# Optimization experiments

Hardware: AMD Instinct MI355X
Metric: run time of the kernel (lower is better)

## Reference

```python
import jax, jax.numpy as jnp
import numpy as np

A, B, OBS, ACT, E, H = 8, 32768, 128, 32, 128, 4
D = E // H  # attend_dim = 32
EPS = 1e-5


def setup_inputs() -> dict:
    key = jax.random.key(0)
    ks = jax.random.split(key, 20)
    std = 0.02
    inp = {
        "observation_vector": jax.random.normal(ks[0], (A, B, OBS), jnp.float32),
        "action_vector": jax.random.uniform(ks[1], (A, B, ACT), jnp.float32),
        # per-agent BatchNorm affine params (torch default init would be 1/0; the
        # module re-inits everything N(0, 0.02), we just use standard BN init)
        "g_gamma": jnp.ones((A, OBS + ACT), jnp.float32),
        "g_beta": jnp.zeros((A, OBS + ACT), jnp.float32),
        "Wg": jax.random.normal(ks[2], (A, OBS + ACT, E), jnp.float32) * std,
        "bg": jnp.zeros((A, E), jnp.float32),
        "s_gamma": jnp.ones((A, OBS), jnp.float32),
        "s_beta": jnp.zeros((A, OBS), jnp.float32),
        "Ws": jax.random.normal(ks[3], (A, OBS, E), jnp.float32) * std,
        "bs": jnp.zeros((A, E), jnp.float32),
        # per-head attention projections (no bias)
        "Wq": jax.random.normal(ks[4], (H, E, D), jnp.float32) * std,
        "Wk": jax.random.normal(ks[5], (H, E, D), jnp.float32) * std,
        "Wv": jax.random.normal(ks[6], (H, E, D), jnp.float32) * std,
        # per-agent f-functions: Linear(2E -> E), LeakyReLU, Linear(E -> ACT)
        "Wf1": jax.random.normal(ks[7], (A, 2 * E, E), jnp.float32) * std,
        "bf1": jnp.zeros((A, E), jnp.float32),
        "Wf2": jax.random.normal(ks[8], (A, E, ACT), jnp.float32) * std,
        "bf2": jnp.zeros((A, ACT), jnp.float32),
    }
    return inp


def _bn(x, gamma, beta):
    # training-mode BatchNorm1d per agent: normalize over batch axis (axis=1)
    mean = x.mean(axis=1, keepdims=True)
    var = x.var(axis=1, keepdims=True)  # biased variance, as torch BN forward
    return (x - mean) * jax.lax.rsqrt(var + EPS) * gamma[:, None, :] + beta[:, None, :]


def reference(observation_vector, action_vector, g_gamma, g_beta, Wg, bg,
              s_gamma, s_beta, Ws, bs, Wq, Wk, Wv, Wf1, bf1, Wf2, bf2):
    lrelu = jax.nn.leaky_relu  # slope 0.01, matches torch default

    combined = jnp.concatenate([observation_vector, action_vector], axis=2)  # [A,B,OBS+ACT]
    e = lrelu(jnp.einsum('abf,afe->abe', _bn(combined, g_gamma, g_beta), Wg) + bg[:, None, :])  # [A,B,E]
    s = lrelu(jnp.einsum('abf,afe->abe', _bn(observation_vector, s_gamma, s_beta), Ws) + bs[:, None, :])  # [A,B,E]

    # per-head projections for all agents at once
    q = jnp.einsum('abe,hed->ahbd', e, Wq)          # [A,H,B,D]
    k = jnp.einsum('abe,hed->ahbd', e, Wk)          # [A,H,B,D]
    v = lrelu(jnp.einsum('abe,hed->ahbd', e, Wv))   # [A,H,B,D]

    # unnormalized scores alpha[i,j] = <k_j, q_i>/sqrt(D) (NO softmax in original)
    alpha = jnp.einsum('ihbd,jhbd->ijhb', q, k) / np.sqrt(D)  # [A,A,H,B]
    mask = 1.0 - jnp.eye(A, dtype=alpha.dtype)                 # exclude j == i
    total = jnp.einsum('ijhb,jhbd->ihbd', alpha * mask[:, :, None, None], v)  # [A,H,B,D]
    xi = jnp.transpose(total, (0, 2, 1, 3)).reshape(A, B, H * D)  # heads concatenated -> [A,B,E]

    fin = jnp.concatenate([xi, s], axis=2)  # [A,B,2E]
    h1 = lrelu(jnp.einsum('abf,afe->abe', fin, Wf1) + bf1[:, None, :])
    all_action_q = jnp.einsum('abe,aec->abc', h1, Wf2) + bf2[:, None, :]  # [A,B,ACT]

    action_ids = jnp.argmax(action_vector, axis=2)  # [A,B]
    curr_action_q = jnp.take_along_axis(all_action_q, action_ids[:, :, None], axis=2)  # [A,B,1]
    return curr_action_q
```

## Files before the change

### kernel.cpp

```cpp
#include <hip/hip_runtime.h>

#define A_ 8
#define B_ 32768
#define OBS_ 128
#define ACT_ 32
#define F_ 160
#define E_ 128
#define H_ 4
#define D_ 32
#define NB_ 16

typedef __attribute__((ext_vector_type(8))) short s16x8;
typedef __attribute__((ext_vector_type(4))) float f32x4;

__device__ __forceinline__ float bf2f(ushort u) {
    union { uint i; float f; } v; v.i = ((uint)u) << 16; return v.f;
}
__device__ __forceinline__ ushort f2bf(float x) {
    union { float f; uint i; } v; v.f = x;
    return (ushort)((v.i + 0x7FFF + ((v.i >> 16) & 1)) >> 16);
}
__device__ __forceinline__ float lrelu(float x) { return x > 0.f ? x : 0.01f * x; }

#define MFMA16(a, b, c) __builtin_amdgcn_mfma_f32_16x16x32_bf16((a), (b), (c), 0, 0, 0)

#define WSB_GSUM   0
#define WSB_GSQ    5120
#define WSB_MEAN   10240
#define WSB_RSTD   15360
#define WSB_BG2    20480
#define WSB_BS2    24576
#define WSB_WGT    28672
#define WSB_WSTH   356352
#define WSB_WSTL   618496
#define WSB_WQT    880640
#define WSB_WKT    913408
#define WSB_WVT    946176
#define WSB_WF1T   978944
#define WSB_WF1TL  1503232
#define WSB_WF2T   1765376
#define WSB_TOTAL  1896448

#define SLOT(m)     ((m) * 9728)
#define XHI(m,r,c)  (SLOT(m) + (r) * 336 + (c) * 2)
#define XLO(m,r,c)  (SLOT(m) + 5376 + (r) * 272 + (c) * 2)
#define SHI(m,r,c)  (SLOT(m) + (r) * 272 + (c) * 2)
#define SLO(m,r,c)  (SLOT(m) + 4352 + (r) * 272 + (c) * 2)
#define OFF_E   77824
#define EA(R,c) (OFF_E + (R) * 272 + (c) * 2)
#define OFF_V   112640
#define VA(R,c) (OFF_V + (R) * 256 + (c) * 2)
#define OFF_QH  145920
#define OFF_KH  150272
#define OFF_AL  154624
#define OFF_BI  162816
#define OFF_PART 163328
#define SMEM_BYTES 163840
__device__ __forceinline__ int qswz(int R, int cb) {
    int a = R * 32 + cb; return a ^ (((R >> 4) & 7) << 4);
}

__global__ void k_zero(float* __restrict__ p) {
    const int i = blockIdx.x * 256 + threadIdx.x;
    if (i < 2560) p[i] = 0.f;
}

__global__ __launch_bounds__(256) void k_stats(const float* __restrict__ obs,
                                               const float* __restrict__ act,
                                               float* __restrict__ gsum,
                                               float* __restrict__ gsq) {
    const int a = blockIdx.y;
    const int b0 = blockIdx.x * (B_ / 64);
    const int tid = threadIdx.x;
    __shared__ float red[256][8];

    {
        const int c = tid & 31, rg = tid >> 5;
        const float4* src = (const float4*)(obs + (size_t)a * B_ * OBS_);
        float4 s = make_float4(0.f,0.f,0.f,0.f), q = make_float4(0.f,0.f,0.f,0.f);
        for (int b = b0 + rg; b < b0 + 512; b += 8) {
            float4 v = src[(size_t)b * 32 + c];
            s.x += v.x; s.y += v.y; s.z += v.z; s.w += v.w;
            q.x += v.x*v.x; q.y += v.y*v.y; q.z += v.z*v.z; q.w += v.w*v.w;
        }
        red[tid][0]=s.x; red[tid][1]=s.y; red[tid][2]=s.z; red[tid][3]=s.w;
        red[tid][4]=q.x; red[tid][5]=q.y; red[tid][6]=q.z; red[tid][7]=q.w;
    }
    __syncthreads();
    if (tid < 128) {
        const int c4 = tid >> 2, j = tid & 3;
        float s = 0.f, q = 0.f;
        #pragma unroll
        for (int rg = 0; rg < 8; rg++) { s += red[rg*32 + c4][j]; q += red[rg*32 + c4][4 + j]; }
        atomicAdd(&gsum[a * F_ + tid], s);
        atomicAdd(&gsq [a * F_ + tid], q);
    }
    __syncthreads();
    {
        const int c = tid & 7, rg = tid >> 3;
        const float4* src = (const float4*)(act + (size_t)a * B_ * ACT_);
        float4 s = make_float4(0.f,0.f,0.f,0.f), q = make_float4(0.f,0.f,0.f,0.f);
        for (int b = b0 + rg; b < b0 + 512; b += 32) {
            float4 v = src[(size_t)b * 8 + c];
            s.x += v.x; s.y += v.y; s.z += v.z; s.w += v.w;
            q.x += v.x*v.x; q.y += v.y*v.y; q.z += v.z*v.z; q.w += v.w*v.w;
        }
        red[tid][0]=s.x; red[tid][1]=s.y; red[tid][2]=s.z; red[tid][3]=s.w;
        red[tid][4]=q.x; red[tid][5]=q.y; red[tid][6]=q.z; red[tid][7]=q.w;
    }
    __syncthreads();
    if (tid < 32) {
        const int c4 = tid >> 2, j = tid & 3;
        float s = 0.f, q = 0.f;
        #pragma unroll
        for (int rg = 0; rg < 32; rg++) { s += red[rg*8 + c4][j]; q += red[rg*8 + c4][4 + j]; }
        atomicAdd(&gsum[a * F_ + 128 + tid], s);
        atomicAdd(&gsq [a * F_ + 128 + tid], q);
    }
}

__global__ void k_finalize(const float* __restrict__ gsum, const float* __restrict__ gsq,
                           float* __restrict__ mean, float* __restrict__ rstd) {
    const int i = blockIdx.x * 256 + threadIdx.x;
    if (i < A_ * F_) {
        const float m = gsum[i] * (1.0f / B_);
        const float v = gsq[i] * (1.0f / B_) - m * m;
        mean[i] = m;
        rstd[i] = rsqrtf(v + 1e-5f);
    }
}

__global__ void k_fold_bias(const float* __restrict__ W, const float* __restrict__ gamma,
                            const float* __restrict__ beta, const float* __restrict__ bias,
                            const float* __restrict__ mean, const float* __restrict__ rstd,
                            float* __restrict__ b2, int F) {
    const int a = blockIdx.x;
    const int c = threadIdx.x;
    float acc = bias[a * E_ + c];
    for (int f = 0; f < F; f++) {
        const float coef = beta[a * F + f] - mean[a * F_ + f] * rstd[a * F_ + f] * gamma[a * F + f];
        acc += coef * W[((size_t)a * F + f) * E_ + c];
    }
    b2[a * E_ + c] = acc;
}

__global__ void k_prep_wgT(const float* __restrict__ Wg, const float* __restrict__ gg,
                           const float* __restrict__ rstd, ushort* __restrict__ WgT) {
    int i = blockIdx.x * 256 + threadIdx.x;
    if (i >= 8 * 128 * 160) return;
    int a = i / (128 * 160), rest = i % (128 * 160);
    int n = rest / 160, k = rest % 160;
    float w = Wg[((size_t)a * 160 + k) * 128 + n] * gg[a * 160 + k] * rstd[a * 160 + k];
    WgT[i] = f2bf(w);
}
__global__ void k_prep_wsT(const float* __restrict__ Ws, const float* __restrict__ sg,
                           const float* __restrict__ rstd,
                           ushort* __restrict__ Th, ushort* __restrict__ Tl) {
    int i = blockIdx.x * 256 + threadIdx.x;
    if (i >= 8 * 128 * 128) return;
    int a = i / (128 * 128), rest = i % (128 * 128);
    int n = rest / 128, k = rest % 128;
    float w = Ws[((size_t)a * 128 + k) * 128 + n] * sg[a * 128 + k] * rstd[a * 160 + k];
    ushort h = f2bf(w);
    Th[i] = h;
    Tl[i] = f2bf(w - bf2f(h));
}
__global__ void k_prep_qkvT(const float* __restrict__ Wq, const float* __restrict__ Wk,
                            const float* __restrict__ Wv, ushort* __restrict__ Tq,
                            ushort* __restrict__ Tk, ushort* __restrict__ Tv) {
    int i = blockIdx.x * 256 + threadIdx.x;
    if (i >= 4 * 32 * 128) return;
    int h = i / (32 * 128), rest = i % (32 * 128);
    int d = rest / 128, e = rest % 128;
    size_t src = ((size_t)h * 128 + e) * 32 + d;
    Tq[i] = f2bf(Wq[src]); Tk[i] = f2bf(Wk[src]); Tv[i] = f2bf(Wv[src]);
}
__global__ void k_prep_f1T(const float* __restrict__ Wf1, ushort* __restrict__ Th,
                           ushort* __restrict__ Tl) {
    int i = blockIdx.x * 256 + threadIdx.x;
    if (i >= 8 * 128 * 256) return;
    int a = i / (128 * 256), rest = i % (128 * 256);
    int n = rest / 256, k = rest % 256;
    float w = Wf1[((size_t)a * 256 + k) * 128 + n];
    ushort h = f2bf(w);
    Th[i] = h;
    if (k >= 128) Tl[((size_t)(a * 128 + n)) * 128 + (k - 128)] = f2bf(w - bf2f(h));
}
__global__ void k_prep_f2T(const float* __restrict__ Wf2, float* __restrict__ T) {
    int i = blockIdx.x * 256 + threadIdx.x;
    if (i >= 8 * 32 * 128) return;
    int a = i / (32 * 128), rest = i % (32 * 128);
    int c = rest / 128, k = rest % 128;
    T[i] = Wf2[((size_t)a * 128 + k) * 32 + c];
}

__global__ __launch_bounds__(512, 1) void k_fused(
    const float* __restrict__ obs, const float* __restrict__ act,
    const ushort* __restrict__ WgT, const float* __restrict__ bg2,
    const ushort* __restrict__ WsTh, const ushort* __restrict__ WsTl,
    const float* __restrict__ bs2,
    const ushort* __restrict__ WqT, const ushort* __restrict__ WkT,
    const ushort* __restrict__ WvT,
    const ushort* __restrict__ Wf1T, const ushort* __restrict__ Wf1Tl,
    const float* __restrict__ bf1,
    const float* __restrict__ Wf2T, const float* __restrict__ bfc2,
    float* __restrict__ out) {
    extern __shared__ char smc[];
    const int tid = threadIdx.x;
    const int b0 = blockIdx.x * NB_;
    const int lane = tid & 63, wv = tid >> 6;
    const int l16 = lane & 15, l4 = lane >> 4;

    {
        const int R = tid >> 2, q = tid & 3;
        const int a = R >> 4, r = R & 15;
        const float* ap = act + ((size_t)a * B_ + b0 + r) * 32 + q * 8;
        float bv = -1e30f; int bi = 0;
        #pragma unroll
        for (int u = 0; u < 8; u++) { float x = ap[u]; if (x > bv) { bv = x; bi = q * 8 + u; } }
        #pragma unroll
        for (int off = 1; off < 4; off <<= 1) {
            float ov = __shfl_xor(bv, off, 4);
            int   oi = __shfl_xor(bi, off, 4);
            if (ov > bv || (ov == bv && oi < bi)) { bv = ov; bi = oi; }
        }
        if (q == 0) *(int*)(smc + OFF_BI + R * 4) = bi;
    }

    for (int i = tid; i < 4096; i += 512) {
        const int R = i >> 5, c4 = i & 31;
        const int a = R >> 4, r = R & 15;
        float4 v = *(const float4*)(obs + ((size_t)a * B_ + b0 + r) * 128 + c4 * 4);
        float vv[4] = {v.x, v.y, v.z, v.w};
        #pragma unroll
        for (int j = 0; j < 4; j++) {
            ushort h = f2bf(vv[j]);
            *(ushort*)(smc + XHI(a, r, c4 * 4 + j)) = h;
            *(ushort*)(smc + XLO(a, r, c4 * 4 + j)) = f2bf(vv[j] - bf2f(h));
        }
    }
    for (int i = tid; i < 1024; i += 512) {
        const int R = i >> 3, c4 = i & 7;
        const int a = R >> 4, r = R & 15;
        float4 v = *(const float4*)(act + ((size_t)a * B_ + b0 + r) * 32 + c4 * 4);
        float vv[4] = {v.x, v.y, v.z, v.w};
        #pragma unroll
        for (int j = 0; j < 4; j++)
            *(ushort*)(smc + XHI(a, r, 128 + c4 * 4 + j)) = f2bf(vv[j]);
    }
    __syncthreads();

    const int n = wv * 16 + l16;

    {
        f32x4 acc[8];
        #pragma unroll
        for (int m = 0; m < 8; m++) acc[m] = (f32x4){0.f, 0.f, 0.f, 0.f};
        #pragma unroll
        for (int kc = 0; kc < 5; kc++) {
            const int kof = kc * 32 + l4 * 8;
            #pragma unroll
            for (int m = 0; m < 8; m++) {
                s16x8 a = *(const s16x8*)(smc + XHI(m, l16, kof));
                s16x8 b = *(const s16x8*)(WgT + ((size_t)m * 128 + n) * 160 + kof);
                acc[m] = MFMA16(a, b, acc[m]);
            }
        }
        #pragma unroll
        for (int m = 0; m < 8; m++) {
            const float bb = bg2[m * 128 + n];
            #pragma unroll
            for (int j = 0; j < 4; j++)
                *(ushort*)(smc + EA(m * 16 + l4 * 4 + j, n)) = f2bf(lrelu(acc[m][j] + bb));
        }
    }
    __syncthreads();

    for (int m = 0; m < 8; m++) {
        f32x4 acc = (f32x4){0.f, 0.f, 0.f, 0.f};
        #pragma unroll
        for (int kc = 0; kc < 4; kc++) {
            const int kof = kc * 32 + l4 * 8;
            s16x8 ah = *(const s16x8*)(smc + XHI(m, l16, kof));
            s16x8 al = *(const s16x8*)(smc + XLO(m, l16, kof));
            s16x8 bh = *(const s16x8*)(WsTh + ((size_t)m * 128 + n) * 128 + kof);
            s16x8 bl = *(const s16x8*)(WsTl + ((size_t)m * 128 + n) * 128 + kof);
            acc = MFMA16(ah, bh, acc);
            acc = MFMA16(al, bh, acc);
            acc = MFMA16(ah, bl, acc);
        }
        __syncthreads();
        const float bb = bs2[m * 128 + n];
        #pragma unroll
        for (int j = 0; j < 4; j++) {
            float s = lrelu(acc[j] + bb);
            ushort h = f2bf(s);
            *(ushort*)(smc + SHI(m, l4 * 4 + j, n)) = h;
            *(ushort*)(smc + SLO(m, l4 * 4 + j, n)) = f2bf(s - bf2f(h));
        }
    }

    {
        f32x4 acc[8];
        #pragma unroll
        for (int m = 0; m < 8; m++) acc[m] = (f32x4){0.f, 0.f, 0.f, 0.f};
        const int h = n >> 5, dl = n & 31;
        const ushort* wp = WvT + ((size_t)(h * 32 + dl)) * 128;
        #pragma unroll
        for (int kc = 0; kc < 4; kc++) {
            const int kof = kc * 32 + l4 * 8;
            s16x8 b = *(const s16x8*)(wp + kof);
            #pragma unroll
            for (int m = 0; m < 8; m++) {
                s16x8 a = *(const s16x8*)(smc + EA(m * 16 + l16, kof));
                acc[m] = MFMA16(a, b, acc[m]);
            }
        }
        #pragma unroll
        for (int m = 0; m < 8; m++)
            #pragma unroll
            for (int j = 0; j < 4; j++)
                *(ushort*)(smc + VA(m * 16 + l4 * 4 + j, n)) = f2bf(lrelu(acc[m][j]));
    }

    float da0 = 0.f, da1 = 0.f;
    for (int hh = 0; hh < 8; hh++) {
        const int h = hh >> 1, dh = hh & 1;
        {
            f32x4 aq = (f32x4){0.f, 0.f, 0.f, 0.f}, ak = (f32x4){0.f, 0.f, 0.f, 0.f};
            const int dl = dh * 16 + l16;
            const ushort* wq = WqT + ((size_t)(h * 32 + dl)) * 128;
            const ushort* wk = WkT + ((size_t)(h * 32 + dl)) * 128;
            #pragma unroll
            for (int kc = 0; kc < 4; kc++) {
                const int kof = kc * 32 + l4 * 8;
                s16x8 a  = *(const s16x8*)(smc + EA(wv * 16 + l16, kof));
                s16x8 bq = *(const s16x8*)(wq + kof);
                s16x8 bk = *(const s16x8*)(wk + kof);
                aq = MFMA16(a, bq, aq);
                ak = MFMA16(a, bk, ak);
            }
            __syncthreads();
            #pragma unroll
            for (int j = 0; j < 4; j++) {
                const int R = wv * 16 + l4 * 4 + j;
                *(ushort*)(smc + OFF_QH + qswz(R, l16 * 2)) = f2bf(aq[j]);
                *(ushort*)(smc + OFF_KH + qswz(R, l16 * 2)) = f2bf(ak[j]);
            }
        }
        __syncthreads();
        #pragma unroll
        for (int p = 0; p < 2; p++) {
            const int e = p * 512 + tid;
            const int j = e & 7, i = (e >> 3) & 7, r = e >> 6;
            const int Rq = i * 16 + r, Rk = j * 16 + r;
            s16x8 q0 = *(const s16x8*)(smc + OFF_QH + qswz(Rq, 0));
            s16x8 q1 = *(const s16x8*)(smc + OFF_QH + qswz(Rq, 16));
            s16x8 k0 = *(const s16x8*)(smc + OFF_KH + qswz(Rk, 0));
            s16x8 k1 = *(const s16x8*)(smc + OFF_KH + qswz(Rk, 16));
            float d = 0.f;
            #pragma unroll
            for (int u = 0; u < 8; u++) d += bf2f((ushort)q0[u]) * bf2f((ushort)k0[u]);
            #pragma unroll
            for (int u = 0; u < 8; u++) d += bf2f((ushort)q1[u]) * bf2f((ushort)k1[u]);
            float& da = p ? da1 : da0;
            if (dh == 0) da = d;
            else {
                const float tot = da + d;
                *(ushort*)(smc + OFF_AL + ((h * 16 + r) * 64 + i * 8 + j) * 2) =
                    (i == j) ? (ushort)0 : f2bf(tot * 0.17677669529663687f);
            }
        }
    }
    __syncthreads();

    for (int m = 0; m < 8; m++) {
        {
            const int c = tid & 127, rg = tid >> 7;
            const int h = c >> 5;
            #pragma unroll
            for (int rr = 0; rr < 4; rr++) {
                const int r = rg * 4 + rr;
                float acc = 0.f;
                #pragma unroll
                for (int j = 0; j < 8; j++) {
                    const float al = bf2f(*(const ushort*)(smc + OFF_AL + ((h * 16 + r) * 64 + m * 8 + j) * 2));
                    const float vv = bf2f(*(const ushort*)(smc + VA(j * 16 + r, c)));
                    acc += al * vv;
                }
                *(ushort*)(smc + EA(r, c)) = f2bf(acc);
            }
        }
        __syncthreads();
        {
            f32x4 acc = (f32x4){0.f, 0.f, 0.f, 0.f};
            const ushort* w1  = Wf1T  + ((size_t)m * 128 + n) * 256;
            const ushort* w1l = Wf1Tl + ((size_t)m * 128 + n) * 128;
            #pragma unroll
            for (int kc = 0; kc < 4; kc++) {
                const int kof = kc * 32 + l4 * 8;
                s16x8 a = *(const s16x8*)(smc + EA(l16, kof));
                s16x8 b = *(const s16x8*)(w1 + kof);
                acc = MFMA16(a, b, acc);
            }
            #pragma unroll
            for (int kc = 0; kc < 4; kc++) {
                const int kof = kc * 32 + l4 * 8;
                s16x8 ah = *(const s16x8*)(smc + SHI(m, l16, kof));
                s16x8 al = *(const s16x8*)(smc + SLO(m, l16, kof));
                s16x8 bh = *(const s16x8*)(w1 + 128 + kof);
                s16x8 bl = *(const s16x8*)(w1l + kof);
                acc = MFMA16(ah, bh, acc);
                acc = MFMA16(al, bh, acc);
                acc = MFMA16(ah, bl, acc);
            }
            const float bb = bf1[m * 128 + n];
            float ps[4];
            #pragma unroll
            for (int j = 0; j < 4; j++) {
                const int r = l4 * 4 + j;
                const int bi = *(const int*)(smc + OFF_BI + (m * 16 + r) * 4);
                const float w2 = Wf2T[((size_t)m * 32 + bi) * 128 + n];
                ps[j] = lrelu(acc[j] + bb) * w2;
            }
            #pragma unroll
            for (int off = 1; off < 16; off <<= 1)
                #pragma unroll
                for (int j = 0; j < 4; j++) ps[j] += __shfl_xor(ps[j], off, 16);
            if (l16 == 0)
                #pragma unroll
                for (int j = 0; j < 4; j++)
                    *(float*)(smc + OFF_PART + ((l4 * 4 + j) * 8 + wv) * 4) = ps[j];
        }
        __syncthreads();
        if (tid < 16) {
            float o = 0.f;
            #pragma unroll
            for (int w = 0; w < 8; w++) o += *(const float*)(smc + OFF_PART + (tid * 8 + w) * 4);
            const int bi = *(const int*)(smc + OFF_BI + (m * 16 + tid) * 4);
            out[(size_t)m * B_ + b0 + tid] = o + bfc2[m * 32 + bi];
        }
        __syncthreads();
    }
}

extern "C" void kernel_launch(void* const* d_in, const int* in_sizes, int n_in,
                              void* d_out, int out_size, void* d_ws, size_t ws_size,
                              hipStream_t stream) {
    const float* obs     = (const float*)d_in[0];
    const float* act     = (const float*)d_in[1];
    const float* g_gamma = (const float*)d_in[2];
    const float* g_beta  = (const float*)d_in[3];
    const float* Wg      = (const float*)d_in[4];
    const float* bg      = (const float*)d_in[5];
    const float* s_gamma = (const float*)d_in[6];
    const float* s_beta  = (const float*)d_in[7];
    const float* Ws      = (const float*)d_in[8];
    const float* bs      = (const float*)d_in[9];
    const float* Wq      = (const float*)d_in[10];
    const float* Wk      = (const float*)d_in[11];
    const float* Wv      = (const float*)d_in[12];
    const float* Wf1     = (const float*)d_in[13];
    const float* bf1     = (const float*)d_in[14];
    const float* Wf2     = (const float*)d_in[15];
    const float* bf2     = (const float*)d_in[16];

    if (ws_size < (size_t)WSB_TOTAL) return;

    (void)hipFuncSetAttribute((const void*)k_fused,
                              hipFuncAttributeMaxDynamicSharedMemorySize, SMEM_BYTES);

    char* ws = (char*)d_ws;
    float*  gsum  = (float*)(ws + WSB_GSUM);
    float*  gsq   = (float*)(ws + WSB_GSQ);
    float*  mean  = (float*)(ws + WSB_MEAN);
    float*  rstd  = (float*)(ws + WSB_RSTD);
    float*  bg2   = (float*)(ws + WSB_BG2);
    float*  bs2   = (float*)(ws + WSB_BS2);
    ushort* WgT   = (ushort*)(ws + WSB_WGT);
    ushort* WsTh  = (ushort*)(ws + WSB_WSTH);
    ushort* WsTl  = (ushort*)(ws + WSB_WSTL);
    ushort* WqT   = (ushort*)(ws + WSB_WQT);
    ushort* WkT   = (ushort*)(ws + WSB_WKT);
    ushort* WvT   = (ushort*)(ws + WSB_WVT);
    ushort* Wf1T  = (ushort*)(ws + WSB_WF1T);
    ushort* Wf1Tl = (ushort*)(ws + WSB_WF1TL);
    float*  Wf2T  = (float*)(ws + WSB_WF2T);

    k_zero<<<10, 256, 0, stream>>>(gsum);
    k_stats<<<dim3(64, A_), 256, 0, stream>>>(obs, act, gsum, gsq);
    k_finalize<<<5, 256, 0, stream>>>(gsum, gsq, mean, rstd);
    k_fold_bias<<<A_, 128, 0, stream>>>(Wg, g_gamma, g_beta, bg, mean, rstd, bg2, F_);
    k_fold_bias<<<A_, 128, 0, stream>>>(Ws, s_gamma, s_beta, bs, mean, rstd, bs2, OBS_);
    k_prep_wgT<<<640, 256, 0, stream>>>(Wg, g_gamma, rstd, WgT);
    k_prep_wsT<<<512, 256, 0, stream>>>(Ws, s_gamma, rstd, WsTh, WsTl);
    k_prep_qkvT<<<64, 256, 0, stream>>>(Wq, Wk, Wv, WqT, WkT, WvT);
    k_prep_f1T<<<1024, 256, 0, stream>>>(Wf1, Wf1T, Wf1Tl);
    k_prep_f2T<<<128, 256, 0, stream>>>(Wf2, Wf2T);
    k_fused<<<B_ / NB_, 512, SMEM_BYTES, stream>>>(
        obs, act, WgT, bg2, WsTh, WsTl, bs2, WqT, WkT, WvT,
        Wf1T, Wf1Tl, bf1, Wf2T, bf2, (float*)d_out);
}
```

Measured before the change: 1.048 ms.

## Restructure fused kernel: merge embedding GEMMs, per-head QK, per-agent f-layer ownership

Merges the Wg and Ws embedding GEMMs into a single pass over the shared input tiles, and computes Q/K one head at a time into swizzled shared buffers so all attention scores are built before aggregation. The value aggregation then runs in one pass, and each wave owns one agent for the f1/f2 layers, so output reductions stay within the wave and per-agent block barriers go away. It also spreads the batch-stats kernel over four times as many blocks. The restructuring trades extra registers (eight held accumulators) and new swizzle layouts for fewer __syncthreads and less redundant shared-memory traffic.

```diff
diff --git a/kernel.cpp b/kernel.cpp
--- a/kernel.cpp
+++ b/kernel.cpp
@@ -44,20 +44,23 @@
 #define SLOT(m)     ((m) * 9728)
 #define XHI(m,r,c)  (SLOT(m) + (r) * 336 + (c) * 2)
 #define XLO(m,r,c)  (SLOT(m) + 5376 + (r) * 272 + (c) * 2)
-#define SHI(m,r,c)  (SLOT(m) + (r) * 272 + (c) * 2)
-#define SLO(m,r,c)  (SLOT(m) + 4352 + (r) * 272 + (c) * 2)
-#define OFF_E   77824
-#define EA(R,c) (OFF_E + (R) * 272 + (c) * 2)
+#define SHI(m,r,c)  ((m) * 8704 + (r) * 272 + (c) * 2)
+#define SLO(m,r,c)  ((m) * 8704 + 4352 + (r) * 272 + (c) * 2)
+#define AL2(h,r,i,j) (69632 + ((((h) * 16 + (r)) * 8 + (i)) * 8 + (j)) * 2)
+#define EA(R,c)     (77824 + (R) * 272 + (c) * 2)
 #define OFF_V   112640
-#define VA(R,c) (OFF_V + (R) * 256 + (c) * 2)
-#define OFF_QH  145920
-#define OFF_KH  150272
-#define OFF_AL  154624
-#define OFF_BI  162816
-#define OFF_PART 163328
-#define SMEM_BYTES 163840
-__device__ __forceinline__ int qswz(int R, int cb) {
-    int a = R * 32 + cb; return a ^ (((R >> 4) & 7) << 4);
+#define OFF_QH  145408
+#define OFF_KH  153600
+#define OFF_BI  161792
+#define SMEM_BYTES 162304
+__device__ __forceinline__ int VA2(int R, int c) {
+    return OFF_V + R * 256 + ((((c >> 3) ^ (R >> 4)) & 15) << 4) + ((c & 7) << 1);
+}
+__device__ __forceinline__ int QHA(int a, int r, int ch) {
+    return OFF_QH + ((((a) * 16 + (r)) * 4 + (((ch) ^ (a)) & 3)) << 4);
+}
+__device__ __forceinline__ int KHA(int a, int r, int ch) {
+    return OFF_KH + ((((a) * 16 + (r)) * 4 + (((ch) ^ (a)) & 3)) << 4);
 }
 
 __global__ void k_zero(float* __restrict__ p) {
@@ -70,7 +73,7 @@
                                                float* __restrict__ gsum,
                                                float* __restrict__ gsq) {
     const int a = blockIdx.y;
-    const int b0 = blockIdx.x * (B_ / 64);
+    const int b0 = blockIdx.x * 128;
     const int tid = threadIdx.x;
     __shared__ float red[256][8];
 
@@ -78,7 +81,7 @@
         const int c = tid & 31, rg = tid >> 5;
         const float4* src = (const float4*)(obs + (size_t)a * B_ * OBS_);
         float4 s = make_float4(0.f,0.f,0.f,0.f), q = make_float4(0.f,0.f,0.f,0.f);
-        for (int b = b0 + rg; b < b0 + 512; b += 8) {
+        for (int b = b0 + rg; b < b0 + 128; b += 8) {
             float4 v = src[(size_t)b * 32 + c];
             s.x += v.x; s.y += v.y; s.z += v.z; s.w += v.w;
             q.x += v.x*v.x; q.y += v.y*v.y; q.z += v.z*v.z; q.w += v.w*v.w;
@@ -100,7 +103,7 @@
         const int c = tid & 7, rg = tid >> 3;
         const float4* src = (const float4*)(act + (size_t)a * B_ * ACT_);
         float4 s = make_float4(0.f,0.f,0.f,0.f), q = make_float4(0.f,0.f,0.f,0.f);
-        for (int b = b0 + rg; b < b0 + 512; b += 32) {
+        for (int b = b0 + rg; b < b0 + 128; b += 32) {
             float4 v = src[(size_t)b * 8 + c];
             s.x += v.x; s.y += v.y; s.z += v.z; s.w += v.w;
             q.x += v.x*v.x; q.y += v.y*v.y; q.z += v.z*v.z; q.w += v.w*v.w;
@@ -252,60 +255,78 @@
 
     const int n = wv * 16 + l16;
 
-    {
-        f32x4 acc[8];
-        #pragma unroll
-        for (int m = 0; m < 8; m++) acc[m] = (f32x4){0.f, 0.f, 0.f, 0.f};
-        #pragma unroll
-        for (int kc = 0; kc < 5; kc++) {
-            const int kof = kc * 32 + l4 * 8;
-            #pragma unroll
-            for (int m = 0; m < 8; m++) {
-                s16x8 a = *(const s16x8*)(smc + XHI(m, l16, kof));
-                s16x8 b = *(const s16x8*)(WgT + ((size_t)m * 128 + n) * 160 + kof);
-                acc[m] = MFMA16(a, b, acc[m]);
-            }
-        }
-        #pragma unroll
-        for (int m = 0; m < 8; m++) {
-            const float bb = bg2[m * 128 + n];
-            #pragma unroll
-            for (int j = 0; j < 4; j++)
-                *(ushort*)(smc + EA(m * 16 + l4 * 4 + j, n)) = f2bf(lrelu(acc[m][j] + bb));
-        }
-    }
-    __syncthreads();
-
+    f32x4 sacc[8];
     for (int m = 0; m < 8; m++) {
-        f32x4 acc = (f32x4){0.f, 0.f, 0.f, 0.f};
+        f32x4 ea = (f32x4){0.f, 0.f, 0.f, 0.f};
+        f32x4 sa = (f32x4){0.f, 0.f, 0.f, 0.f};
         #pragma unroll
         for (int kc = 0; kc < 4; kc++) {
             const int kof = kc * 32 + l4 * 8;
             s16x8 ah = *(const s16x8*)(smc + XHI(m, l16, kof));
             s16x8 al = *(const s16x8*)(smc + XLO(m, l16, kof));
+            s16x8 bg = *(const s16x8*)(WgT + ((size_t)m * 128 + n) * 160 + kof);
             s16x8 bh = *(const s16x8*)(WsTh + ((size_t)m * 128 + n) * 128 + kof);
             s16x8 bl = *(const s16x8*)(WsTl + ((size_t)m * 128 + n) * 128 + kof);
-            acc = MFMA16(ah, bh, acc);
-            acc = MFMA16(al, bh, acc);
-            acc = MFMA16(ah, bl, acc);
-        }
-        __syncthreads();
+            ea = MFMA16(ah, bg, ea);
+            sa = MFMA16(ah, bh, sa);
+            sa = MFMA16(al, bh, sa);
+            sa = MFMA16(ah, bl, sa);
+        }
+        {
+            const int kof = 128 + l4 * 8;
+            s16x8 ah = *(const s16x8*)(smc + XHI(m, l16, kof));
+            s16x8 bg = *(const s16x8*)(WgT + ((size_t)m * 128 + n) * 160 + kof);
+            ea = MFMA16(ah, bg, ea);
+        }
+        const float bb = bg2[m * 128 + n];
+        #pragma unroll
+        for (int j = 0; j < 4; j++)
+            *(ushort*)(smc + EA(m * 16 + l4 * 4 + j, n)) = f2bf(lrelu(ea[j] + bb));
+        sacc[m] = sa;
+    }
+    __syncthreads();
+    #pragma unroll
+    for (int m = 0; m < 8; m++) {
         const float bb = bs2[m * 128 + n];
         #pragma unroll
         for (int j = 0; j < 4; j++) {
-            float s = lrelu(acc[j] + bb);
+            float s = lrelu(sacc[m][j] + bb);
             ushort h = f2bf(s);
             *(ushort*)(smc + SHI(m, l4 * 4 + j, n)) = h;
             *(ushort*)(smc + SLO(m, l4 * 4 + j, n)) = f2bf(s - bf2f(h));
         }
     }
+    __syncthreads();
+
+    auto qk_head = [&](int h) {
+        #pragma unroll
+        for (int dt = 0; dt < 2; dt++) {
+            f32x4 aq = (f32x4){0.f, 0.f, 0.f, 0.f};
+            f32x4 ak = (f32x4){0.f, 0.f, 0.f, 0.f};
+            const int d = dt * 16 + l16;
+            const ushort* wq = WqT + ((size_t)(h * 32 + d)) * 128;
+            const ushort* wk = WkT + ((size_t)(h * 32 + d)) * 128;
+            #pragma unroll
+            for (int kc = 0; kc < 4; kc++) {
+                const int kof = kc * 32 + l4 * 8;
+                s16x8 a  = *(const s16x8*)(smc + EA(wv * 16 + l16, kof));
+                aq = MFMA16(a, *(const s16x8*)(wq + kof), aq);
+                ak = MFMA16(a, *(const s16x8*)(wk + kof), ak);
+            }
+            #pragma unroll
+            for (int j = 0; j < 4; j++) {
+                const int r = l4 * 4 + j;
+                *(ushort*)(smc + QHA(wv, r, d >> 3) + (d & 7) * 2) = f2bf(aq[j]);
+                *(ushort*)(smc + KHA(wv, r, d >> 3) + (d & 7) * 2) = f2bf(ak[j]);
+            }
+        }
+    };
 
     {
         f32x4 acc[8];
         #pragma unroll
         for (int m = 0; m < 8; m++) acc[m] = (f32x4){0.f, 0.f, 0.f, 0.f};
-        const int h = n >> 5, dl = n & 31;
-        const ushort* wp = WvT + ((size_t)(h * 32 + dl)) * 128;
+        const ushort* wp = WvT + ((size_t)n) * 128;
         #pragma unroll
         for (int kc = 0; kc < 4; kc++) {
             const int kof = kc * 32 + l4 * 8;
@@ -320,88 +341,68 @@
         for (int m = 0; m < 8; m++)
             #pragma unroll
             for (int j = 0; j < 4; j++)
-                *(ushort*)(smc + VA(m * 16 + l4 * 4 + j, n)) = f2bf(lrelu(acc[m][j]));
-    }
-
-    float da0 = 0.f, da1 = 0.f;
-    for (int hh = 0; hh < 8; hh++) {
-        const int h = hh >> 1, dh = hh & 1;
-        {
-            f32x4 aq = (f32x4){0.f, 0.f, 0.f, 0.f}, ak = (f32x4){0.f, 0.f, 0.f, 0.f};
-            const int dl = dh * 16 + l16;
-            const ushort* wq = WqT + ((size_t)(h * 32 + dl)) * 128;
-            const ushort* wk = WkT + ((size_t)(h * 32 + dl)) * 128;
-            #pragma unroll
-            for (int kc = 0; kc < 4; kc++) {
-                const int kof = kc * 32 + l4 * 8;
-                s16x8 a  = *(const s16x8*)(smc + EA(wv * 16 + l16, kof));
-                s16x8 bq = *(const s16x8*)(wq + kof);
-                s16x8 bk = *(const s16x8*)(wk + kof);
-                aq = MFMA16(a, bq, aq);
-                ak = MFMA16(a, bk, ak);
-            }
-            __syncthreads();
-            #pragma unroll
-            for (int j = 0; j < 4; j++) {
-                const int R = wv * 16 + l4 * 4 + j;
-                *(ushort*)(smc + OFF_QH + qswz(R, l16 * 2)) = f2bf(aq[j]);
-                *(ushort*)(smc + OFF_KH + qswz(R, l16 * 2)) = f2bf(ak[j]);
-            }
-        }
-        __syncthreads();
+                *(ushort*)(smc + VA2(m * 16 + l4 * 4 + j, n)) = f2bf(lrelu(acc[m][j]));
+    }
+    qk_head(0);
+    __syncthreads();
+
+    for (int h = 0; h < 4; h++) {
         #pragma unroll
         for (int p = 0; p < 2; p++) {
             const int e = p * 512 + tid;
             const int j = e & 7, i = (e >> 3) & 7, r = e >> 6;
-            const int Rq = i * 16 + r, Rk = j * 16 + r;
-            s16x8 q0 = *(const s16x8*)(smc + OFF_QH + qswz(Rq, 0));
-            s16x8 q1 = *(const s16x8*)(smc + OFF_QH + qswz(Rq, 16));
-            s16x8 k0 = *(const s16x8*)(smc + OFF_KH + qswz(Rk, 0));
-            s16x8 k1 = *(const s16x8*)(smc + OFF_KH + qswz(Rk, 16));
-            float d = 0.f;
-            #pragma unroll
-            for (int u = 0; u < 8; u++) d += bf2f((ushort)q0[u]) * bf2f((ushort)k0[u]);
-            #pragma unroll
-            for (int u = 0; u < 8; u++) d += bf2f((ushort)q1[u]) * bf2f((ushort)k1[u]);
-            float& da = p ? da1 : da0;
-            if (dh == 0) da = d;
-            else {
-                const float tot = da + d;
-                *(ushort*)(smc + OFF_AL + ((h * 16 + r) * 64 + i * 8 + j) * 2) =
-                    (i == j) ? (ushort)0 : f2bf(tot * 0.17677669529663687f);
-            }
-        }
-    }
-    __syncthreads();
-
-    for (int m = 0; m < 8; m++) {
-        {
-            const int c = tid & 127, rg = tid >> 7;
-            const int h = c >> 5;
-            #pragma unroll
-            for (int rr = 0; rr < 4; rr++) {
-                const int r = rg * 4 + rr;
-                float acc = 0.f;
+            float dot = 0.f;
+            #pragma unroll
+            for (int ch = 0; ch < 4; ch++) {
+                s16x8 qv = *(const s16x8*)(smc + QHA(i, r, ch));
+                s16x8 kv = *(const s16x8*)(smc + KHA(j, r, ch));
                 #pragma unroll
-                for (int j = 0; j < 8; j++) {
-                    const float al = bf2f(*(const ushort*)(smc + OFF_AL + ((h * 16 + r) * 64 + m * 8 + j) * 2));
-                    const float vv = bf2f(*(const ushort*)(smc + VA(j * 16 + r, c)));
-                    acc += al * vv;
-                }
-                *(ushort*)(smc + EA(r, c)) = f2bf(acc);
-            }
+                for (int u = 0; u < 8; u++)
+                    dot += bf2f((ushort)qv[u]) * bf2f((ushort)kv[u]);
+            }
+            *(ushort*)(smc + AL2(h, r, i, j)) =
+                (i == j) ? (ushort)0 : f2bf(dot * 0.17677669529663687f);
         }
         __syncthreads();
-        {
+        if (h < 3) {
+            qk_head(h + 1);
+            __syncthreads();
+        }
+    }
+
+    {
+        const int c = tid & 127, rg = tid >> 7;
+        const int h = c >> 5;
+        for (int rr = 0; rr < 32; rr++) {
+            const int R = rg * 32 + rr;
+            const int a = R >> 4, r = R & 15;
+            s16x8 av = *(const s16x8*)(smc + AL2(h, r, a, 0));
+            float acc = 0.f;
+            #pragma unroll
+            for (int j = 0; j < 8; j++)
+                acc += bf2f((ushort)av[j]) * bf2f(*(const ushort*)(smc + VA2(j * 16 + r, c)));
+            *(ushort*)(smc + EA(R, c)) = f2bf(acc);
+        }
+    }
+    __syncthreads();
+
+    {
+        const int m = wv;
+        float ps[4] = {0.f, 0.f, 0.f, 0.f};
+        int bis[4];
+        #pragma unroll
+        for (int j = 0; j < 4; j++)
+            bis[j] = *(const int*)(smc + OFF_BI + (m * 16 + l4 * 4 + j) * 4);
+        for (int nt = 0; nt < 8; nt++) {
+            const int nn = nt * 16 + l16;
             f32x4 acc = (f32x4){0.f, 0.f, 0.f, 0.f};
-            const ushort* w1  = Wf1T  + ((size_t)m * 128 + n) * 256;
-            const ushort* w1l = Wf1Tl + ((size_t)m * 128 + n) * 128;
+            const ushort* w1  = Wf1T  + ((size_t)m * 128 + nn) * 256;
+            const ushort* w1l = Wf1Tl + ((size_t)m * 128 + nn) * 128;
             #pragma unroll
             for (int kc = 0; kc < 4; kc++) {
                 const int kof = kc * 32 + l4 * 8;
-                s16x8 a = *(const s16x8*)(smc + EA(l16, kof));
-                s16x8 b = *(const s16x8*)(w1 + kof);
-                acc = MFMA16(a, b, acc);
+                s16x8 a = *(const s16x8*)(smc + EA(m * 16 + l16, kof));
+                acc = MFMA16(a, *(const s16x8*)(w1 + kof), acc);
             }
             #pragma unroll
             for (int kc = 0; kc < 4; kc++) {
@@ -414,33 +415,21 @@
                 acc = MFMA16(al, bh, acc);
                 acc = MFMA16(ah, bl, acc);
             }
-            const float bb = bf1[m * 128 + n];
-            float ps[4];
+            const float bb = bf1[m * 128 + nn];
             #pragma unroll
             for (int j = 0; j < 4; j++) {
-                const int r = l4 * 4 + j;
-                const int bi = *(const int*)(smc + OFF_BI + (m * 16 + r) * 4);
-                const float w2 = Wf2T[((size_t)m * 32 + bi) * 128 + n];
-                ps[j] = lrelu(acc[j] + bb) * w2;
-            }
-            #pragma unroll
-            for (int off = 1; off < 16; off <<= 1)
-                #pragma unroll
-                for (int j = 0; j < 4; j++) ps[j] += __shfl_xor(ps[j], off, 16);
-            if (l16 == 0)
-                #pragma unroll
-                for (int j = 0; j < 4; j++)
-                    *(float*)(smc + OFF_PART + ((l4 * 4 + j) * 8 + wv) * 4) = ps[j];
-        }
-        __syncthreads();
-        if (tid < 16) {
-            float o = 0.f;
-            #pragma unroll
-            for (int w = 0; w < 8; w++) o += *(const float*)(smc + OFF_PART + (tid * 8 + w) * 4);
-            const int bi = *(const int*)(smc + OFF_BI + (m * 16 + tid) * 4);
-            out[(size_t)m * B_ + b0 + tid] = o + bfc2[m * 32 + bi];
-        }
-        __syncthreads();
+                const float w2 = Wf2T[((size_t)m * 32 + bis[j]) * 128 + nn];
+                ps[j] += lrelu(acc[j] + bb) * w2;
+            }
+        }
+        #pragma unroll
+        for (int off = 1; off < 16; off <<= 1)
+            #pragma unroll
+            for (int j = 0; j < 4; j++) ps[j] += __shfl_xor(ps[j], off, 16);
+        if (l16 == 0)
+            #pragma unroll
+            for (int j = 0; j < 4; j++)
+                out[(size_t)m * B_ + b0 + l4 * 4 + j] = ps[j] + bfc2[m * 32 + bis[j]];
     }
 }
 
@@ -488,7 +477,7 @@
     float*  Wf2T  = (float*)(ws + WSB_WF2T);
 
     k_zero<<<10, 256, 0, stream>>>(gsum);
-    k_stats<<<dim3(64, A_), 256, 0, stream>>>(obs, act, gsum, gsq);
+    k_stats<<<dim3(256, A_), 256, 0, stream>>>(obs, act, gsum, gsq);
     k_finalize<<<5, 256, 0, stream>>>(gsum, gsq, mean, rstd);
     k_fold_bias<<<A_, 128, 0, stream>>>(Wg, g_gamma, g_beta, bg, mean, rstd, bg2, F_);
     k_fold_bias<<<A_, 128, 0, stream>>>(Ws, s_gamma, s_beta, bs, mean, rstd, bs2, OBS_);
```

After: 953.0 us. 1.1x faster.
